# Optimization experiments

Measured on AMD Instinct MI355X. Metric: run time of the kernel, lower is better.

The kernel has to match this reference:

```python
import jax, jax.numpy as jnp
import numpy as np

FP8_MAX = 448.0


def setup_inputs() -> dict:
    key = jax.random.key(0)
    kx, kw = jax.random.split(key)
    in_features, out_features = 1024, 1024
    x = jax.random.normal(kx, (32768, in_features), dtype=jnp.float32)
    # kaiming_uniform_ with a=sqrt(5): bound = sqrt(6/((1+a^2)*fan_in)) = sqrt(1/fan_in)
    bound = 1.0 / np.sqrt(in_features)
    weight = jax.random.uniform(kw, (out_features, in_features), dtype=jnp.float32,
                                minval=-bound, maxval=bound)
    bias = jnp.zeros((out_features,), dtype=jnp.float32)
    return {"x": x, "weight": weight, "bias": bias}


def reference(x, weight, bias):
    # per-tensor input quant
    input_scale = jnp.maximum(jnp.max(jnp.abs(x)) / FP8_MAX, 1e-12)
    x_q = jnp.round(jnp.clip(x / input_scale, -FP8_MAX, FP8_MAX))
    # per-output-channel weight quant
    weight_amax = jnp.max(jnp.abs(weight), axis=1)            # [out]
    weight_scale = jnp.maximum(weight_amax / FP8_MAX, 1e-12)  # [out]
    weight_q = jnp.round(jnp.clip(weight / weight_scale[:, None], -FP8_MAX, FP8_MAX))
    # integer-valued GEMM in fp32, then dequant + bias
    output_q = jnp.einsum('ti,oi->to', x_q, weight_q)          # [T, out]
    output = output_q * (input_scale * weight_scale)[None, :]
    return output + bias
```

## Files before the change

kernel.cpp:

```cpp
#include <hip/hip_runtime.h>
#include <hip/hip_fp16.h>

#define FP8_MAX 448.0f
#define M_ 32768
#define N_ 1024
#define K_ 1024
#define BM 128
#define BN 128
#define BK 64

typedef _Float16 f16x8 __attribute__((ext_vector_type(8)));
typedef _Float16 f16x4 __attribute__((ext_vector_type(4)));
typedef __fp16  h16x2 __attribute__((ext_vector_type(2)));
typedef float f32x16 __attribute__((ext_vector_type(16)));

__device__ inline void gload_lds16(const void* g, void* l) {
    __builtin_amdgcn_global_load_lds(
        (const __attribute__((address_space(1))) void*)g,
        (__attribute__((address_space(3))) void*)l,
        16, 0, 0);
}

__device__ inline f16x8 quant8(float4 v0, float4 v1, float inv) {
    h16x2 t0 = __builtin_amdgcn_cvt_pkrtz(rintf(v0.x * inv), rintf(v0.y * inv));
    h16x2 t1 = __builtin_amdgcn_cvt_pkrtz(rintf(v0.z * inv), rintf(v0.w * inv));
    h16x2 t2 = __builtin_amdgcn_cvt_pkrtz(rintf(v1.x * inv), rintf(v1.y * inv));
    h16x2 t3 = __builtin_amdgcn_cvt_pkrtz(rintf(v1.z * inv), rintf(v1.w * inv));
    f16x8 q;
    q[0] = (_Float16)t0[0]; q[1] = (_Float16)t0[1];
    q[2] = (_Float16)t1[0]; q[3] = (_Float16)t1[1];
    q[4] = (_Float16)t2[0]; q[5] = (_Float16)t2[1];
    q[6] = (_Float16)t3[0]; q[7] = (_Float16)t3[1];
    return q;
}

__device__ inline void mfma_tile(const _Float16* sAb, const _Float16* sBb,
                                 f32x16 acc[2][2],
                                 int wm, int wn, int m32, int m7, int h) {
    #pragma unroll
    for (int ks = 0; ks < 4; ++ks) {
        f16x8 a[2], b[2];
        const int chunk = ks * 2 + h;
        const int pos = (chunk ^ m7) * 8;
        #pragma unroll
        for (int i = 0; i < 2; ++i)
            a[i] = *(const f16x8*)&sAb[(wm + i * 32 + m32) * BK + pos];
        #pragma unroll
        for (int j = 0; j < 2; ++j)
            b[j] = *(const f16x8*)&sBb[(wn + j * 32 + m32) * BK + pos];
        #pragma unroll
        for (int i = 0; i < 2; ++i)
            #pragma unroll
            for (int j = 0; j < 2; ++j)
                acc[i][j] = __builtin_amdgcn_mfma_f32_32x32x16_f16(a[i], b[j], acc[i][j], 0, 0, 0);
    }
}

__global__ __launch_bounds__(256) void prep_kernel(const float* __restrict__ x,
                                                   const float* __restrict__ w,
                                                   float* __restrict__ xamax_part,
                                                   float* __restrict__ wscale,
                                                   _Float16* __restrict__ wq,
                                                   int n) {
    __shared__ float sm[4];
    if (blockIdx.x < 1024) {
        int row = blockIdx.x;
        const float4* wr4 = (const float4*)(w + (size_t)row * K_);
        float4 v = wr4[threadIdx.x];
        float m = fmaxf(fmaxf(fabsf(v.x), fabsf(v.y)), fmaxf(fabsf(v.z), fabsf(v.w)));
        #pragma unroll
        for (int off = 32; off > 0; off >>= 1)
            m = fmaxf(m, __shfl_down(m, off, 64));
        if ((threadIdx.x & 63) == 0) sm[threadIdx.x >> 6] = m;
        __syncthreads();
        m = fmaxf(fmaxf(sm[0], sm[1]), fmaxf(sm[2], sm[3]));
        float scale = fmaxf(m / FP8_MAX, 1e-12f);
        if (threadIdx.x == 0) wscale[row] = scale;
        float inv = 1.0f / scale;
        f16x4 o;
        o[0] = (_Float16)rintf(fminf(fmaxf(v.x * inv, -FP8_MAX), FP8_MAX));
        o[1] = (_Float16)rintf(fminf(fmaxf(v.y * inv, -FP8_MAX), FP8_MAX));
        o[2] = (_Float16)rintf(fminf(fmaxf(v.z * inv, -FP8_MAX), FP8_MAX));
        o[3] = (_Float16)rintf(fminf(fmaxf(v.w * inv, -FP8_MAX), FP8_MAX));
        ((f16x4*)(wq + (size_t)row * K_))[threadIdx.x] = o;
    } else {
        float m = 0.0f;
        const float4* x4 = (const float4*)x;
        int n4 = n >> 2;
        int stride = 2048 * 256;
        for (int i = (blockIdx.x - 1024) * 256 + threadIdx.x; i < n4; i += stride) {
            float4 v = x4[i];
            m = fmaxf(m, fmaxf(fmaxf(fabsf(v.x), fabsf(v.y)),
                               fmaxf(fabsf(v.z), fabsf(v.w))));
        }
        #pragma unroll
        for (int off = 32; off > 0; off >>= 1)
            m = fmaxf(m, __shfl_down(m, off, 64));
        if ((threadIdx.x & 63) == 0) sm[threadIdx.x >> 6] = m;
        __syncthreads();
        if (threadIdx.x == 0) {
            xamax_part[blockIdx.x - 1024] =
                fmaxf(fmaxf(sm[0], sm[1]), fmaxf(sm[2], sm[3]));
        }
    }
}

__global__ __launch_bounds__(256) void gemm_kernel(const float* __restrict__ x,
                                                   const _Float16* __restrict__ wq,
                                                   const float* __restrict__ xamax_part,
                                                   const float* __restrict__ wscale,
                                                   const float* __restrict__ bias,
                                                   float* __restrict__ out) {
    __shared__ __align__(16) _Float16 sA[2][BM * BK];
    __shared__ __align__(16) _Float16 sB[2][BN * BK];

    const int tid = threadIdx.x;
    const int wave = tid >> 6;
    const int lane = tid & 63;
    const int h   = lane >> 5;
    const int m32 = lane & 31;
    const int m7  = m32 & 7;
    const int wm = (wave >> 1) * 64;
    const int wn = (wave & 1) * 64;

    const int bb = (int)blockIdx.x;
    const int n0 = ((bb >> 3) & 7) * BN;
    const int m0 = (((bb >> 6) << 3) + (bb & 7)) * BM;

    const int trow = tid >> 3;
    const int tcol = (((tid & 7) ^ (trow & 7)) * 8);
    const _Float16* Bg = wq + ((size_t)(n0 + trow)) * K_ + tcol;
    char* lB0 = (char*)&sB[0][0] + wave * 1024;
    char* lB1 = (char*)&sB[1][0] + wave * 1024;

    const int arow = tid >> 3;
    const int ach  = tid & 7;
    const float* Ag = x + (size_t)(m0 + arow) * K_ + ach * 8;
    _Float16* Aw0 = &sA[0][0] + (size_t)arow * BK + ((ach ^ (arow & 7)) * 8);
    _Float16* Aw1 = Aw0 + BM * BK;

    float4 pvA[4][2], pvB[4][2];

    #pragma unroll
    for (int rr = 0; rr < 4; ++rr)
        gload_lds16(Bg + (size_t)(rr * 32) * K_, lB0 + rr * 4096);
    #pragma unroll
    for (int rr = 0; rr < 4; ++rr) {
        const float* src = Ag + (size_t)(rr * 32) * K_;
        pvA[rr][0] = *(const float4*)src;
        pvA[rr][1] = *(const float4*)(src + 4);
    }

    const float4* p4 = (const float4*)xamax_part;
    float4 pa = p4[tid];
    float4 pb = p4[tid + 256];
    float m = fmaxf(fmaxf(fmaxf(pa.x, pa.y), fmaxf(pa.z, pa.w)),
                    fmaxf(fmaxf(pb.x, pb.y), fmaxf(pb.z, pb.w)));
    #pragma unroll
    for (int off = 32; off > 0; off >>= 1)
        m = fmaxf(m, __shfl_down(m, off, 64));
    float* red = (float*)&sA[0][0];
    if ((tid & 63) == 0) red[tid >> 6] = m;
    __syncthreads();
    const float amax = fmaxf(fmaxf(red[0], red[1]), fmaxf(red[2], red[3]));
    __syncthreads();
    const float iscale = fmaxf(amax / FP8_MAX, 1e-12f);
    const float inv = 1.0f / iscale;

    #pragma unroll
    for (int rr = 0; rr < 4; ++rr)
        *(f16x8*)(Aw0 + (size_t)(rr * 32) * BK) = quant8(pvA[rr][0], pvA[rr][1], inv);
    #pragma unroll
    for (int rr = 0; rr < 4; ++rr) {
        const float* src = Ag + BK + (size_t)(rr * 32) * K_;
        pvB[rr][0] = *(const float4*)src;
        pvB[rr][1] = *(const float4*)(src + 4);
    }

    f32x16 acc[2][2] = {};

    for (int kt = 0; kt < K_; kt += 2 * BK) {
        __syncthreads();
        #pragma unroll
        for (int rr = 0; rr < 4; ++rr)
            gload_lds16(Bg + (kt + BK) + (size_t)(rr * 32) * K_, lB1 + rr * 4096);
        {
            const int kA = (kt + 2 * BK) & (K_ - 1);
            #pragma unroll
            for (int rr = 0; rr < 4; ++rr) {
                const float* src = Ag + kA + (size_t)(rr * 32) * K_;
                pvA[rr][0] = *(const float4*)src;
                pvA[rr][1] = *(const float4*)(src + 4);
            }
        }
        asm volatile("" ::: "memory");
        mfma_tile(&sA[0][0], &sB[0][0], acc, wm, wn, m32, m7, h);
        #pragma unroll
        for (int rr = 0; rr < 4; ++rr)
            *(f16x8*)(Aw1 + (size_t)(rr * 32) * BK) = quant8(pvB[rr][0], pvB[rr][1], inv);

        __syncthreads();
        {
            const int kB = (kt + 2 * BK) & (K_ - 1);
            #pragma unroll
            for (int rr = 0; rr < 4; ++rr)
                gload_lds16(Bg + kB + (size_t)(rr * 32) * K_, lB0 + rr * 4096);
            const int kA = (kt + 3 * BK) & (K_ - 1);
            #pragma unroll
            for (int rr = 0; rr < 4; ++rr) {
                const float* src = Ag + kA + (size_t)(rr * 32) * K_;
                pvB[rr][0] = *(const float4*)src;
                pvB[rr][1] = *(const float4*)(src + 4);
            }
        }
        asm volatile("" ::: "memory");
        mfma_tile(&sA[1][0], &sB[1][0], acc, wm, wn, m32, m7, h);
        #pragma unroll
        for (int rr = 0; rr < 4; ++rr)
            *(f16x8*)(Aw0 + (size_t)(rr * 32) * BK) = quant8(pvA[rr][0], pvA[rr][1], inv);
    }

    #pragma unroll
    for (int j = 0; j < 2; ++j) {
        int col = n0 + wn + j * 32 + m32;
        float sc = iscale * wscale[col];
        float bs = bias[col];
        #pragma unroll
        for (int i = 0; i < 2; ++i) {
            int rb = m0 + wm + i * 32 + 4 * h;
            #pragma unroll
            for (int reg = 0; reg < 16; ++reg) {
                int row = rb + (reg & 3) + 8 * (reg >> 2);
                out[(size_t)row * N_ + col] = acc[i][j][reg] * sc + bs;
            }
        }
    }
}

extern "C" void kernel_launch(void* const* d_in, const int* in_sizes, int n_in,
                              void* d_out, int out_size, void* d_ws, size_t ws_size,
                              hipStream_t stream) {
    const float* x    = (const float*)d_in[0];
    const float* w    = (const float*)d_in[1];
    const float* bias = (const float*)d_in[2];
    float* out = (float*)d_out;

    char* ws = (char*)d_ws;
    float* xamax_part  = (float*)(ws + 1024);
    float* wscale      = (float*)(ws + 16384);
    _Float16* wq       = (_Float16*)(ws + 32768);

    prep_kernel<<<3072, 256, 0, stream>>>(x, w, xamax_part, wscale, wq, M_ * K_);
    gemm_kernel<<<2048, 256, 0, stream>>>(x, wq, xamax_part, wscale, bias, out);
}
```

Before: 319.9 us.

## Single-buffer quantized A tile in LDS and skip wasted tail prefetches

Drops the double buffer for the quantized A tile in shared memory, keeping one A buffer, which cuts LDS use per block by 16 KB. This may allow more resident blocks per CU. In exchange each k-step now needs extra barriers around the A-tile rewrite, so quantize-and-store no longer overlaps with the MFMA on the other buffer. It also guards out the wrapped-around prefetches of x and weight past the end of K.

```diff
diff --git a/kernel.cpp b/kernel.cpp
--- a/kernel.cpp
+++ b/kernel.cpp
@@ -111,7 +111,7 @@
                                                    const float* __restrict__ wscale,
                                                    const float* __restrict__ bias,
                                                    float* __restrict__ out) {
-    __shared__ __align__(16) _Float16 sA[2][BM * BK];
+    __shared__ __align__(16) _Float16 sA[BM * BK];
     __shared__ __align__(16) _Float16 sB[2][BN * BK];
 
     const int tid = threadIdx.x;
@@ -136,8 +136,7 @@
     const int arow = tid >> 3;
     const int ach  = tid & 7;
     const float* Ag = x + (size_t)(m0 + arow) * K_ + ach * 8;
-    _Float16* Aw0 = &sA[0][0] + (size_t)arow * BK + ((ach ^ (arow & 7)) * 8);
-    _Float16* Aw1 = Aw0 + BM * BK;
+    _Float16* Aw = sA + (size_t)arow * BK + ((ach ^ (arow & 7)) * 8);
 
     float4 pvA[4][2], pvB[4][2];
 
@@ -159,7 +158,7 @@
     #pragma unroll
     for (int off = 32; off > 0; off >>= 1)
         m = fmaxf(m, __shfl_down(m, off, 64));
-    float* red = (float*)&sA[0][0];
+    float* red = (float*)sA;
     if ((tid & 63) == 0) red[tid >> 6] = m;
     __syncthreads();
     const float amax = fmaxf(fmaxf(red[0], red[1]), fmaxf(red[2], red[3]));
@@ -169,55 +168,59 @@
 
     #pragma unroll
     for (int rr = 0; rr < 4; ++rr)
-        *(f16x8*)(Aw0 + (size_t)(rr * 32) * BK) = quant8(pvA[rr][0], pvA[rr][1], inv);
+        *(f16x8*)(Aw + (size_t)(rr * 32) * BK) = quant8(pvA[rr][0], pvA[rr][1], inv);
     #pragma unroll
     for (int rr = 0; rr < 4; ++rr) {
         const float* src = Ag + BK + (size_t)(rr * 32) * K_;
         pvB[rr][0] = *(const float4*)src;
         pvB[rr][1] = *(const float4*)(src + 4);
     }
+    __syncthreads();
 
     f32x16 acc[2][2] = {};
 
     for (int kt = 0; kt < K_; kt += 2 * BK) {
-        __syncthreads();
         #pragma unroll
         for (int rr = 0; rr < 4; ++rr)
             gload_lds16(Bg + (kt + BK) + (size_t)(rr * 32) * K_, lB1 + rr * 4096);
-        {
-            const int kA = (kt + 2 * BK) & (K_ - 1);
+        if (kt + 2 * BK < K_) {
             #pragma unroll
             for (int rr = 0; rr < 4; ++rr) {
-                const float* src = Ag + kA + (size_t)(rr * 32) * K_;
+                const float* src = Ag + (kt + 2 * BK) + (size_t)(rr * 32) * K_;
                 pvA[rr][0] = *(const float4*)src;
                 pvA[rr][1] = *(const float4*)(src + 4);
             }
         }
         asm volatile("" ::: "memory");
-        mfma_tile(&sA[0][0], &sB[0][0], acc, wm, wn, m32, m7, h);
+        mfma_tile(sA, &sB[0][0], acc, wm, wn, m32, m7, h);
+        __syncthreads();
         #pragma unroll
         for (int rr = 0; rr < 4; ++rr)
-            *(f16x8*)(Aw1 + (size_t)(rr * 32) * BK) = quant8(pvB[rr][0], pvB[rr][1], inv);
-
-        __syncthreads();
-        {
-            const int kB = (kt + 2 * BK) & (K_ - 1);
+            *(f16x8*)(Aw + (size_t)(rr * 32) * BK) = quant8(pvB[rr][0], pvB[rr][1], inv);
+        __syncthreads();
+
+        if (kt + 2 * BK < K_) {
             #pragma unroll
             for (int rr = 0; rr < 4; ++rr)
-                gload_lds16(Bg + kB + (size_t)(rr * 32) * K_, lB0 + rr * 4096);
-            const int kA = (kt + 3 * BK) & (K_ - 1);
+                gload_lds16(Bg + (kt + 2 * BK) + (size_t)(rr * 32) * K_, lB0 + rr * 4096);
+        }
+        if (kt + 3 * BK < K_) {
             #pragma unroll
             for (int rr = 0; rr < 4; ++rr) {
-                const float* src = Ag + kA + (size_t)(rr * 32) * K_;
+                const float* src = Ag + (kt + 3 * BK) + (size_t)(rr * 32) * K_;
                 pvB[rr][0] = *(const float4*)src;
                 pvB[rr][1] = *(const float4*)(src + 4);
             }
         }
         asm volatile("" ::: "memory");
-        mfma_tile(&sA[1][0], &sB[1][0], acc, wm, wn, m32, m7, h);
-        #pragma unroll
-        for (int rr = 0; rr < 4; ++rr)
-            *(f16x8*)(Aw0 + (size_t)(rr * 32) * BK) = quant8(pvA[rr][0], pvA[rr][1], inv);
+        mfma_tile(sA, &sB[1][0], acc, wm, wn, m32, m7, h);
+        if (kt + 2 * BK < K_) {
+            __syncthreads();
+            #pragma unroll
+            for (int rr = 0; rr < 4; ++rr)
+                *(f16x8*)(Aw + (size_t)(rr * 32) * BK) = quant8(pvA[rr][0], pvA[rr][1], inv);
+            __syncthreads();
+        }
     }
 
     #pragma unroll
```

Result: no change. 322.4 us (+0.8%).
